# Optimization experiments

Hardware: AMD Instinct MI355X
Metric: run time of the kernel (lower is better)

The kernel has to match this reference:

```python
import jax, jax.numpy as jnp
import numpy as np

BATCH, N_MACS_PREV, CMS_PREV, NEUR_PREV = 256, 512, 8, 16
FILTER_LEN = 256
NUM_CMS, NUM_NEURONS = 32, 32
NUM_INPUTS = FILTER_LEN * CMS_PREV * NEUR_PREV  # 32768


def setup_inputs() -> dict:
    key = jax.random.key(0)
    k1, k2, k3 = jax.random.split(key, 3)
    x = jax.random.uniform(k1, (BATCH, N_MACS_PREV, CMS_PREV, NEUR_PREV), dtype=jnp.float32)
    input_filter = jax.random.randint(k2, (FILTER_LEN,), 0, N_MACS_PREV)
    # binary {0,1} weights, matching torch.randint(0, 2, ..., dtype=float32)
    weights = jax.random.randint(k3, (NUM_CMS, NUM_INPUTS, NUM_NEURONS), 0, 2).astype(jnp.float32)
    return {"x": x, "input_filter": input_filter, "weights": weights}


def reference(x, input_filter, weights):
    B = x.shape[0]
    # gather receptive field MACs and flatten: (B, num_inputs)
    xg = jnp.take(x, input_filter, axis=1).reshape(B, -1)
    # sum-normalize, nan_to_num handles all-zero rows (0/0 -> 0)
    xn = jnp.nan_to_num(xg / jnp.sum(xg, axis=-1, keepdims=True))
    # batched matmul: (B,I) x (C,I,N) -> (B,C,N)  (torch does (C,B,N) then permutes)
    acts = jnp.einsum('bi,cin->bcn', xn, weights)
    # familiarity-based softmax temperature
    familiarities = jnp.max(acts, axis=-1)          # (B, C)
    avg_fam = jnp.mean(familiarities)               # scalar
    softmax_temp = 1.0 / (avg_fam + 1e-4) - 1.0
    logits = acts / softmax_temp
    # categorical sample per (batch, cm); fixed key for determinism
    samples = jax.random.categorical(jax.random.key(42), logits, axis=-1)  # (B, C)
    # scatter one-hot write-out, int output as in torch
    out = jax.nn.one_hot(samples, NUM_NEURONS, dtype=jnp.int32)  # (B, C, N)
    return out
```

## Files before the change

### kernel.cpp

```cpp
#include <hip/hip_runtime.h>
#include <stdint.h>

#define BATCH 256
#define NMAC  512
#define ROWF  128
#define I_    32768
#define C_    32
#define N_    32
#define XROW  (NMAC * ROWF)
#define NCH   64

typedef float  f32x4  __attribute__((ext_vector_type(4)));
typedef __bf16 bf16x8 __attribute__((ext_vector_type(8)));

__device__ __forceinline__ uint32_t f2bf_rne(float f) {
    uint32_t u = __builtin_bit_cast(uint32_t, f);
    return (u + 0x7FFFu + ((u >> 16) & 1u)) >> 16;
}

__global__ __launch_bounds__(256) void k_sum(const float* __restrict__ x,
                                             const int* __restrict__ filt,
                                             float* __restrict__ S) {
    const int b = blockIdx.x;
    const int t = threadIdx.x;
    const float* xb = x + (size_t)b * XROW;
    float s = 0.f;
    for (int it = 0; it < 32; ++it) {
        int idx4 = it * 256 + t;
        int f = idx4 >> 5;
        int j4 = idx4 & 31;
        float4 v = *(const float4*)(xb + (size_t)filt[f] * ROWF + j4 * 4);
        s += v.x + v.y + v.z + v.w;
    }
    for (int o = 32; o > 0; o >>= 1) s += __shfl_down(s, o, 64);
    __shared__ float red[4];
    if ((t & 63) == 0) red[t >> 6] = s;
    __syncthreads();
    if (t == 0) S[b] = red[0] + red[1] + red[2] + red[3];
}

__global__ __launch_bounds__(256, 2) void k_gemm3(const float* __restrict__ x,
                                                  const int* __restrict__ filt,
                                                  const float* __restrict__ w,
                                                  float* __restrict__ part) {
    __shared__ __align__(16) unsigned short afr[16 * 512];
    __shared__ __align__(16) unsigned short wfr[8 * 512];

    const int t  = threadIdx.x;
    const int l  = t & 63;
    const int wv = t >> 6;
    const int chunk = blockIdx.x & 63;
    const int c0 = ((blockIdx.x >> 6) & 7) * 4;
    const int b0 = (blockIdx.x >> 9) * 128;

    f32x4 acc[2][8];
#pragma unroll
    for (int bt = 0; bt < 2; ++bt)
#pragma unroll
        for (int ct = 0; ct < 8; ++ct) acc[bt][ct] = f32x4{0.f, 0.f, 0.f, 0.f};

    const int ar     = t >> 3;
    const int ai     = t & 7;
    const int a_quad = ai >> 1;
    const int a_j    = (ai & 1) * 4;
    const int wn = t & 31;
    const int wc = t >> 5;

    for (int st = 0; st < 16; ++st) {
        const int ifull = chunk * 512 + st * 32;
        const int fidx  = filt[ifull >> 7];
        const int ioff  = ifull & 127;
        const float* xs = x + (size_t)b0 * XROW + (size_t)fidx * ROWF + ioff;

#pragma unroll
        for (int rr = 0; rr < 4; ++rr) {
            int row = rr * 32 + ar;
            float4 v = *(const float4*)(xs + (size_t)row * XROW + ai * 4);
            uint32_t u0 = __builtin_bit_cast(uint32_t, v.x);
            uint32_t u1 = __builtin_bit_cast(uint32_t, v.y);
            uint32_t u2 = __builtin_bit_cast(uint32_t, v.z);
            uint32_t u3 = __builtin_bit_cast(uint32_t, v.w);
            float l0 = v.x - __builtin_bit_cast(float, u0 & 0xFFFF0000u);
            float l1 = v.y - __builtin_bit_cast(float, u1 & 0xFFFF0000u);
            float l2 = v.z - __builtin_bit_cast(float, u2 & 0xFFFF0000u);
            float l3 = v.w - __builtin_bit_cast(float, u3 & 0xFFFF0000u);
            uint2 hp, lp;
            hp.x = (u0 >> 16) | (u1 & 0xFFFF0000u);
            hp.y = (u2 >> 16) | (u3 & 0xFFFF0000u);
            lp.x = f2bf_rne(l0) | (f2bf_rne(l1) << 16);
            lp.y = f2bf_rne(l2) | (f2bf_rne(l3) << 16);
            int rt   = row >> 4;
            int lane = a_quad * 16 + (row & 15);
            int base = (rt * 2) * 512 + lane * 8 + a_j;
            *(uint2*)&afr[base]       = hp;
            *(uint2*)&afr[base + 512] = lp;
        }

#pragma unroll
        for (int q = 0; q < 8; ++q) {
            int sl  = wc + 8 * q;
            int c   = sl >> 4;
            int il  = (sl & 15) * 2;
            const float* wp = w + ((size_t)(c0 + c) * I_ + ifull + il) * N_ + wn;
            uint32_t u0 = __builtin_bit_cast(uint32_t, wp[0]);
            uint32_t u1 = __builtin_bit_cast(uint32_t, wp[N_]);
            uint32_t pk = (u0 >> 16) | (u1 & 0xFFFF0000u);
            int lane = (il >> 3) * 16 + (wn & 15);
            int ct   = c * 2 + (wn >> 4);
            *(uint32_t*)&wfr[ct * 512 + lane * 8 + (il & 7)] = pk;
        }
        __syncthreads();

        bf16x8 av[2][2];
#pragma unroll
        for (int bt = 0; bt < 2; ++bt)
#pragma unroll
            for (int p = 0; p < 2; ++p)
                av[bt][p] = *(const bf16x8*)&afr[((wv * 2 + bt) * 2 + p) * 512 + l * 8];
        bf16x8 bv[8];
#pragma unroll
        for (int ct = 0; ct < 8; ++ct)
            bv[ct] = *(const bf16x8*)&wfr[ct * 512 + l * 8];
#pragma unroll
        for (int bt = 0; bt < 2; ++bt)
#pragma unroll
            for (int ct = 0; ct < 8; ++ct) {
                acc[bt][ct] = __builtin_amdgcn_mfma_f32_16x16x32_bf16(av[bt][0], bv[ct], acc[bt][ct], 0, 0, 0);
                acc[bt][ct] = __builtin_amdgcn_mfma_f32_16x16x32_bf16(av[bt][1], bv[ct], acc[bt][ct], 0, 0, 0);
            }
        __syncthreads();
    }

    const int quad = l >> 4, n15 = l & 15;
    float* dst = part + (size_t)chunk * (BATCH * C_ * N_);
#pragma unroll
    for (int bt = 0; bt < 2; ++bt) {
#pragma unroll
        for (int ct = 0; ct < 8; ++ct) {
            int c = c0 + (ct >> 1);
            int n = (ct & 1) * 16 + n15;
#pragma unroll
            for (int r = 0; r < 4; ++r) {
                int b = b0 + (wv * 2 + bt) * 16 + quad * 4 + r;
                dst[((size_t)b * C_ + c) * N_ + n] = acc[bt][ct][r];
            }
        }
    }
}

__global__ __launch_bounds__(256, 2) void k_gemm_fb(const float* __restrict__ x,
                                                    const int* __restrict__ filt,
                                                    const float* __restrict__ w,
                                                    float* __restrict__ raw) {
    __shared__ __align__(16) unsigned short afr[32 * 512];
    __shared__ __align__(16) unsigned short wfr[8 * 512];

    const int t  = threadIdx.x;
    const int l  = t & 63;
    const int wv = t >> 6;
    const int chunk = blockIdx.x & 63;
    const int c0 = (blockIdx.x >> 6) * 4;

    f32x4 acc[4][8];
#pragma unroll
    for (int bt = 0; bt < 4; ++bt)
#pragma unroll
        for (int ct = 0; ct < 8; ++ct) acc[bt][ct] = f32x4{0.f, 0.f, 0.f, 0.f};

    const int ar     = t >> 3;
    const int ai     = t & 7;
    const int a_quad = ai >> 1;
    const int a_j    = (ai & 1) * 4;
    const int wn = t & 31;
    const int wc = t >> 5;

    for (int st = 0; st < 16; ++st) {
        const int ifull = chunk * 512 + st * 32;
        const int fidx  = filt[ifull >> 7];
        const int ioff  = ifull & 127;
        const float* xs = x + (size_t)fidx * ROWF + ioff;

#pragma unroll
        for (int rr = 0; rr < 8; ++rr) {
            int row = rr * 32 + ar;
            float4 v = *(const float4*)(xs + (size_t)row * XROW + ai * 4);
            uint32_t u0 = __builtin_bit_cast(uint32_t, v.x);
            uint32_t u1 = __builtin_bit_cast(uint32_t, v.y);
            uint32_t u2 = __builtin_bit_cast(uint32_t, v.z);
            uint32_t u3 = __builtin_bit_cast(uint32_t, v.w);
            float l0 = v.x - __builtin_bit_cast(float, u0 & 0xFFFF0000u);
            float l1 = v.y - __builtin_bit_cast(float, u1 & 0xFFFF0000u);
            float l2 = v.z - __builtin_bit_cast(float, u2 & 0xFFFF0000u);
            float l3 = v.w - __builtin_bit_cast(float, u3 & 0xFFFF0000u);
            uint2 hp, lp;
            hp.x = (u0 >> 16) | (u1 & 0xFFFF0000u);
            hp.y = (u2 >> 16) | (u3 & 0xFFFF0000u);
            lp.x = f2bf_rne(l0) | (f2bf_rne(l1) << 16);
            lp.y = f2bf_rne(l2) | (f2bf_rne(l3) << 16);
            int rt   = row >> 4;
            int lane = a_quad * 16 + (row & 15);
            int base = (rt * 2) * 512 + lane * 8 + a_j;
            *(uint2*)&afr[base]       = hp;
            *(uint2*)&afr[base + 512] = lp;
        }
#pragma unroll
        for (int q = 0; q < 8; ++q) {
            int sl  = wc + 8 * q;
            int c   = sl >> 4;
            int il  = (sl & 15) * 2;
            const float* wp = w + ((size_t)(c0 + c) * I_ + ifull + il) * N_ + wn;
            uint32_t u0 = __builtin_bit_cast(uint32_t, wp[0]);
            uint32_t u1 = __builtin_bit_cast(uint32_t, wp[N_]);
            uint32_t pk = (u0 >> 16) | (u1 & 0xFFFF0000u);
            int lane = (il >> 3) * 16 + (wn & 15);
            int ct   = c * 2 + (wn >> 4);
            *(uint32_t*)&wfr[ct * 512 + lane * 8 + (il & 7)] = pk;
        }
        __syncthreads();

        bf16x8 av[4][2];
#pragma unroll
        for (int bt = 0; bt < 4; ++bt)
#pragma unroll
            for (int p = 0; p < 2; ++p)
                av[bt][p] = *(const bf16x8*)&afr[((wv * 4 + bt) * 2 + p) * 512 + l * 8];
        bf16x8 bv[8];
#pragma unroll
        for (int ct = 0; ct < 8; ++ct)
            bv[ct] = *(const bf16x8*)&wfr[ct * 512 + l * 8];
#pragma unroll
        for (int bt = 0; bt < 4; ++bt)
#pragma unroll
            for (int ct = 0; ct < 8; ++ct) {
                acc[bt][ct] = __builtin_amdgcn_mfma_f32_16x16x32_bf16(av[bt][0], bv[ct], acc[bt][ct], 0, 0, 0);
                acc[bt][ct] = __builtin_amdgcn_mfma_f32_16x16x32_bf16(av[bt][1], bv[ct], acc[bt][ct], 0, 0, 0);
            }
        __syncthreads();
    }

    const int quad = l >> 4, n15 = l & 15;
#pragma unroll
    for (int bt = 0; bt < 4; ++bt)
#pragma unroll
        for (int ct = 0; ct < 8; ++ct) {
            int c = c0 + (ct >> 1);
            int n = (ct & 1) * 16 + n15;
#pragma unroll
            for (int r = 0; r < 4; ++r) {
                int b = (wv * 4 + bt) * 16 + quad * 4 + r;
                atomicAdd(&raw[((size_t)b * C_ + c) * N_ + n], acc[bt][ct][r]);
            }
        }
}

__global__ __launch_bounds__(256) void k_reduce(const float* __restrict__ part,
                                                const float* __restrict__ S,
                                                float* __restrict__ raw,
                                                float* __restrict__ fam) {
    const int i4 = blockIdx.x * 256 + threadIdx.x;
    const f32x4* p = (const f32x4*)part;
    f32x4 s = f32x4{0.f, 0.f, 0.f, 0.f};
#pragma unroll 8
    for (int ch = 0; ch < NCH; ++ch) s += p[(size_t)ch * 65536 + i4];
    ((f32x4*)raw)[i4] = s;
    float m = fmaxf(fmaxf(s[0], s[1]), fmaxf(s[2], s[3]));
    m = fmaxf(m, __shfl_xor(m, 1, 64));
    m = fmaxf(m, __shfl_xor(m, 2, 64));
    m = fmaxf(m, __shfl_xor(m, 4, 64));
    int r = i4 >> 3;
    float v = ((i4 & 7) == 0) ? (m / S[r >> 5]) : 0.f;
    for (int o = 32; o > 0; o >>= 1) v += __shfl_down(v, o, 64);
    __shared__ float red[4];
    if ((threadIdx.x & 63) == 0) red[threadIdx.x >> 6] = v;
    __syncthreads();
    if (threadIdx.x == 0) atomicAdd(fam, red[0] + red[1] + red[2] + red[3]);
}

__global__ __launch_bounds__(256) void k_fam(const float* __restrict__ raw,
                                             const float* __restrict__ S,
                                             float* __restrict__ fam) {
    int r = blockIdx.x * 256 + threadIdx.x;
    const float4* ap = (const float4*)(raw + (size_t)r * N_);
    float m = -3.0e38f;
#pragma unroll
    for (int q = 0; q < 8; ++q) {
        float4 v = ap[q];
        m = fmaxf(m, fmaxf(fmaxf(v.x, v.y), fmaxf(v.z, v.w)));
    }
    m = m / S[r >> 5];
    for (int o = 32; o > 0; o >>= 1) m += __shfl_down(m, o, 64);
    __shared__ float red[4];
    if ((threadIdx.x & 63) == 0) red[threadIdx.x >> 6] = m;
    __syncthreads();
    if (threadIdx.x == 0) atomicAdd(fam, red[0] + red[1] + red[2] + red[3]);
}

__device__ __forceinline__ uint32_t rotl32(uint32_t x, uint32_t r) {
    return (x << r) | (x >> (32u - r));
}
__device__ __forceinline__ void threefry(uint32_t k0, uint32_t k1,
                                         uint32_t x0, uint32_t x1,
                                         uint32_t& o0, uint32_t& o1) {
    uint32_t ks2 = k0 ^ k1 ^ 0x1BD11BDAu;
    x0 += k0; x1 += k1;
    x0 += x1; x1 = rotl32(x1, 13); x1 ^= x0;
    x0 += x1; x1 = rotl32(x1, 15); x1 ^= x0;
    x0 += x1; x1 = rotl32(x1, 26); x1 ^= x0;
    x0 += x1; x1 = rotl32(x1, 6);  x1 ^= x0;
    x0 += k1; x1 += ks2 + 1u;
    x0 += x1; x1 = rotl32(x1, 17); x1 ^= x0;
    x0 += x1; x1 = rotl32(x1, 29); x1 ^= x0;
    x0 += x1; x1 = rotl32(x1, 16); x1 ^= x0;
    x0 += x1; x1 = rotl32(x1, 24); x1 ^= x0;
    x0 += ks2; x1 += k0 + 2u;
    x0 += x1; x1 = rotl32(x1, 13); x1 ^= x0;
    x0 += x1; x1 = rotl32(x1, 15); x1 ^= x0;
    x0 += x1; x1 = rotl32(x1, 26); x1 ^= x0;
    x0 += x1; x1 = rotl32(x1, 6);  x1 ^= x0;
    x0 += k0; x1 += k1 + 3u;
    x0 += x1; x1 = rotl32(x1, 17); x1 ^= x0;
    x0 += x1; x1 = rotl32(x1, 29); x1 ^= x0;
    x0 += x1; x1 = rotl32(x1, 16); x1 ^= x0;
    x0 += x1; x1 = rotl32(x1, 24); x1 ^= x0;
    x0 += k1; x1 += ks2 + 4u;
    x0 += x1; x1 = rotl32(x1, 13); x1 ^= x0;
    x0 += x1; x1 = rotl32(x1, 15); x1 ^= x0;
    x0 += x1; x1 = rotl32(x1, 26); x1 ^= x0;
    x0 += x1; x1 = rotl32(x1, 6);  x1 ^= x0;
    x0 += ks2; x1 += k0 + 5u;
    o0 = x0; o1 = x1;
}

__device__ __forceinline__ float gumbel_of(uint32_t bits) {
    uint32_t fb = (bits >> 9) | 0x3F800000u;
    float f = __builtin_bit_cast(float, fb) - 1.0f;
    float u = f + 1.17549435e-38f;
    return -logf(-logf(u));
}

__global__ __launch_bounds__(256) void k_sample(const float* __restrict__ raw,
                                                const float* __restrict__ S,
                                                const float* __restrict__ fam,
                                                int* __restrict__ out) {
    int r0 = blockIdx.x * 256 + threadIdx.x;
    int r1 = r0 + 4096;
    float avg  = fam[0] * (1.0f / 8192.0f);
    float temp = 1.0f / (avg + 1e-4f) - 1.0f;
    float sA = S[r0 >> 5], sB = S[r1 >> 5];
    const float* apA = raw + (size_t)r0 * N_;
    const float* apB = raw + (size_t)r1 * N_;

    float bestA = -3.4e38f, bestB = -3.4e38f;
    int biA = 0, biB = 0;
    for (int n = 0; n < 32; ++n) {
        uint32_t iA = (uint32_t)(r0 * 32 + n);
        uint32_t iB = (uint32_t)(r1 * 32 + n);
        uint32_t a0, a1, b0, b1;
        threefry(0u, 42u, 0u, iA, a0, a1);
        threefry(0u, 42u, 0u, iB, b0, b1);
        float vA = (apA[n] / sA) / temp + gumbel_of(a0 ^ a1);
        float vB = (apB[n] / sB) / temp + gumbel_of(b0 ^ b1);
        if (vA > bestA) { bestA = vA; biA = n; }
        if (vB > bestB) { bestB = vB; biB = n; }
    }
    int4* opA = (int4*)(out + (size_t)r0 * N_);
    int4* opB = (int4*)(out + (size_t)r1 * N_);
#pragma unroll
    for (int q = 0; q < 8; ++q) {
        int4 a, b;
        a.x = (q * 4 + 0) == biA; a.y = (q * 4 + 1) == biA;
        a.z = (q * 4 + 2) == biA; a.w = (q * 4 + 3) == biA;
        b.x = (q * 4 + 0) == biB; b.y = (q * 4 + 1) == biB;
        b.z = (q * 4 + 2) == biB; b.w = (q * 4 + 3) == biB;
        opA[q] = a; opB[q] = b;
    }
}

extern "C" void kernel_launch(void* const* d_in, const int* in_sizes, int n_in,
                              void* d_out, int out_size, void* d_ws, size_t ws_size,
                              hipStream_t stream) {
    const float* x    = (const float*)d_in[0];
    const int*   filt = (const int*)d_in[1];
    const float* w    = (const float*)d_in[2];
    int* out = (int*)d_out;

    char* ws = (char*)d_ws;
    float* raw  = (float*)ws;
    float* fam  = (float*)(ws + (1 << 20));
    float* S    = (float*)(ws + (1 << 20) + 128);
    float* part = (float*)(ws + (2u << 20));

    const size_t need_part = (2u << 20) + (size_t)NCH * (BATCH * C_ * N_) * sizeof(float);

    if (ws_size >= need_part) {
        hipMemsetAsync(ws + (1 << 20), 0, 128, stream);
        hipLaunchKernelGGL(k_sum,    dim3(256),  dim3(256), 0, stream, x, filt, S);
        hipLaunchKernelGGL(k_gemm3,  dim3(1024), dim3(256), 0, stream, x, filt, w, part);
        hipLaunchKernelGGL(k_reduce, dim3(256),  dim3(256), 0, stream, part, S, raw, fam);
        hipLaunchKernelGGL(k_sample, dim3(16),   dim3(256), 0, stream, raw, S, fam, out);
    } else {
        hipMemsetAsync(ws, 0, (1 << 20) + 128, stream);
        hipLaunchKernelGGL(k_sum,    dim3(256), dim3(256), 0, stream, x, filt, S);
        hipLaunchKernelGGL(k_gemm_fb, dim3(512), dim3(256), 0, stream, x, filt, w, raw);
        hipLaunchKernelGGL(k_fam,    dim3(32),  dim3(256), 0, stream, raw, S, fam);
        hipLaunchKernelGGL(k_sample, dim3(16),  dim3(256), 0, stream, raw, S, fam, out);
    }
}
```

Before: 296.2 us.

## Retile GEMM to full batch per block and prefetch weights into registers

Each GEMM block now covers all 256 batch rows for 2 CMs instead of 128 rows for 4 CMs, so the weight tensor is streamed only once while activations are re-read more often. Weight tiles for the next step are loaded into registers before the current activation conversion, overlapping weight fetch latency with the compute. This trades weight bandwidth for more activation traffic and higher register pressure.

```diff
diff --git a/kernel.cpp b/kernel.cpp
--- a/kernel.cpp
+++ b/kernel.cpp
@@ -39,25 +39,24 @@
     if (t == 0) S[b] = red[0] + red[1] + red[2] + red[3];
 }
 
-__global__ __launch_bounds__(256, 2) void k_gemm3(const float* __restrict__ x,
+__global__ __launch_bounds__(256, 2) void k_gemm4(const float* __restrict__ x,
                                                   const int* __restrict__ filt,
                                                   const float* __restrict__ w,
                                                   float* __restrict__ part) {
-    __shared__ __align__(16) unsigned short afr[16 * 512];
-    __shared__ __align__(16) unsigned short wfr[8 * 512];
+    __shared__ __align__(16) unsigned short afr[32 * 512];
+    __shared__ __align__(16) unsigned short wfr[4 * 512];
 
     const int t  = threadIdx.x;
     const int l  = t & 63;
     const int wv = t >> 6;
     const int chunk = blockIdx.x & 63;
-    const int c0 = ((blockIdx.x >> 6) & 7) * 4;
-    const int b0 = (blockIdx.x >> 9) * 128;
-
-    f32x4 acc[2][8];
-#pragma unroll
-    for (int bt = 0; bt < 2; ++bt)
-#pragma unroll
-        for (int ct = 0; ct < 8; ++ct) acc[bt][ct] = f32x4{0.f, 0.f, 0.f, 0.f};
+    const int c0 = (blockIdx.x >> 6) * 2;
+
+    f32x4 acc[4][4];
+#pragma unroll
+    for (int bt = 0; bt < 4; ++bt)
+#pragma unroll
+        for (int ct = 0; ct < 4; ++ct) acc[bt][ct] = f32x4{0.f, 0.f, 0.f, 0.f};
 
     const int ar     = t >> 3;
     const int ai     = t & 7;
@@ -66,14 +65,45 @@
     const int wn = t & 31;
     const int wc = t >> 5;
 
+    uint32_t Wr[2][4];
+    auto loadW = [&](int st, int sel) {
+        const int ifull = chunk * 512 + st * 32;
+#pragma unroll
+        for (int q = 0; q < 4; ++q) {
+            int sl = wc + 8 * q;
+            int c  = sl >> 4;
+            int il = (sl & 15) * 2;
+            const float* wp = w + ((size_t)(c0 + c) * I_ + ifull + il) * N_ + wn;
+            uint32_t u0 = __builtin_bit_cast(uint32_t, wp[0]);
+            uint32_t u1 = __builtin_bit_cast(uint32_t, wp[N_]);
+            Wr[sel][q] = (u0 >> 16) | (u1 & 0xFFFF0000u);
+        }
+    };
+    auto storeW = [&](int sel) {
+#pragma unroll
+        for (int q = 0; q < 4; ++q) {
+            int sl = wc + 8 * q;
+            int c  = sl >> 4;
+            int il = (sl & 15) * 2;
+            int lane = (il >> 3) * 16 + (wn & 15);
+            int ct   = c * 2 + (wn >> 4);
+            *(uint32_t*)&wfr[ct * 512 + lane * 8 + (il & 7)] = Wr[sel][q];
+        }
+    };
+
+    loadW(0, 0);
     for (int st = 0; st < 16; ++st) {
         const int ifull = chunk * 512 + st * 32;
         const int fidx  = filt[ifull >> 7];
         const int ioff  = ifull & 127;
-        const float* xs = x + (size_t)b0 * XROW + (size_t)fidx * ROWF + ioff;
-
-#pragma unroll
-        for (int rr = 0; rr < 4; ++rr) {
+        const float* xs = x + (size_t)fidx * ROWF + ioff;
+        const int cur = st & 1, nxt = cur ^ 1;
+
+        storeW(cur);
+        if (st + 1 < 16) loadW(st + 1, nxt);
+
+#pragma unroll
+        for (int rr = 0; rr < 8; ++rr) {
             int row = rr * 32 + ar;
             float4 v = *(const float4*)(xs + (size_t)row * XROW + ai * 4);
             uint32_t u0 = __builtin_bit_cast(uint32_t, v.x);
@@ -95,36 +125,22 @@
             *(uint2*)&afr[base]       = hp;
             *(uint2*)&afr[base + 512] = lp;
         }
-
-#pragma unroll
-        for (int q = 0; q < 8; ++q) {
-            int sl  = wc + 8 * q;
-            int c   = sl >> 4;
-            int il  = (sl & 15) * 2;
-            const float* wp = w + ((size_t)(c0 + c) * I_ + ifull + il) * N_ + wn;
-            uint32_t u0 = __builtin_bit_cast(uint32_t, wp[0]);
-            uint32_t u1 = __builtin_bit_cast(uint32_t, wp[N_]);
-            uint32_t pk = (u0 >> 16) | (u1 & 0xFFFF0000u);
-            int lane = (il >> 3) * 16 + (wn & 15);
-            int ct   = c * 2 + (wn >> 4);
-            *(uint32_t*)&wfr[ct * 512 + lane * 8 + (il & 7)] = pk;
-        }
         __syncthreads();
 
-        bf16x8 av[2][2];
-#pragma unroll
-        for (int bt = 0; bt < 2; ++bt)
+        bf16x8 av[4][2];
+#pragma unroll
+        for (int bt = 0; bt < 4; ++bt)
 #pragma unroll
             for (int p = 0; p < 2; ++p)
-                av[bt][p] = *(const bf16x8*)&afr[((wv * 2 + bt) * 2 + p) * 512 + l * 8];
-        bf16x8 bv[8];
-#pragma unroll
-        for (int ct = 0; ct < 8; ++ct)
+                av[bt][p] = *(const bf16x8*)&afr[((wv * 4 + bt) * 2 + p) * 512 + l * 8];
+        bf16x8 bv[4];
+#pragma unroll
+        for (int ct = 0; ct < 4; ++ct)
             bv[ct] = *(const bf16x8*)&wfr[ct * 512 + l * 8];
 #pragma unroll
-        for (int bt = 0; bt < 2; ++bt)
-#pragma unroll
-            for (int ct = 0; ct < 8; ++ct) {
+        for (int bt = 0; bt < 4; ++bt)
+#pragma unroll
+            for (int ct = 0; ct < 4; ++ct) {
                 acc[bt][ct] = __builtin_amdgcn_mfma_f32_16x16x32_bf16(av[bt][0], bv[ct], acc[bt][ct], 0, 0, 0);
                 acc[bt][ct] = __builtin_amdgcn_mfma_f32_16x16x32_bf16(av[bt][1], bv[ct], acc[bt][ct], 0, 0, 0);
             }
@@ -134,14 +150,14 @@
     const int quad = l >> 4, n15 = l & 15;
     float* dst = part + (size_t)chunk * (BATCH * C_ * N_);
 #pragma unroll
-    for (int bt = 0; bt < 2; ++bt) {
-#pragma unroll
-        for (int ct = 0; ct < 8; ++ct) {
+    for (int bt = 0; bt < 4; ++bt) {
+#pragma unroll
+        for (int ct = 0; ct < 4; ++ct) {
             int c = c0 + (ct >> 1);
             int n = (ct & 1) * 16 + n15;
 #pragma unroll
             for (int r = 0; r < 4; ++r) {
-                int b = b0 + (wv * 2 + bt) * 16 + quad * 4 + r;
+                int b = (wv * 4 + bt) * 16 + quad * 4 + r;
                 dst[((size_t)b * C_ + c) * N_ + n] = acc[bt][ct][r];
             }
         }
@@ -395,7 +411,7 @@
     if (ws_size >= need_part) {
         hipMemsetAsync(ws + (1 << 20), 0, 128, stream);
         hipLaunchKernelGGL(k_sum,    dim3(256),  dim3(256), 0, stream, x, filt, S);
-        hipLaunchKernelGGL(k_gemm3,  dim3(1024), dim3(256), 0, stream, x, filt, w, part);
+        hipLaunchKernelGGL(k_gemm4,  dim3(1024), dim3(256), 0, stream, x, filt, w, part);
         hipLaunchKernelGGL(k_reduce, dim3(256),  dim3(256), 0, stream, part, S, raw, fam);
         hipLaunchKernelGGL(k_sample, dim3(16),   dim3(256), 0, stream, raw, S, fam, out);
     } else {
```

Result: slower. 390.4 us (+31.8%).
